# Performance work log

Measured on AMD Instinct MI355X. Metric: run time of the kernel, lower is better.

## Reference

```python
import jax, jax.numpy as jnp
import numpy as np

D = 1024          # d_model / hidden_size
F = 2048          # d_ff / intermediate_size
E = 7             # routed experts = num_experts(8) - num_shared(1)
K = 2             # top_k
AUX_COEF = 0.01


def setup_inputs() -> dict:
    key = jax.random.key(0)
    ks = jax.random.split(key, 6)
    std = 0.02
    x = jax.random.normal(ks[0], (2, 1024, D), dtype=jnp.float32)
    router_w = jax.random.normal(ks[1], (E, D), dtype=jnp.float32) * std      # Linear(D->E), no bias
    cfc_w = jax.random.normal(ks[2], (E, 2 * F, D), dtype=jnp.float32) * std  # fused gate+up per expert
    cproj_w = jax.random.normal(ks[3], (E, D, F), dtype=jnp.float32) * std    # down proj per expert
    shared_fc_w = jax.random.normal(ks[4], (2 * F, D), dtype=jnp.float32) * std
    shared_proj_w = jax.random.normal(ks[5], (D, F), dtype=jnp.float32) * std
    return {"x": x, "router_w": router_w, "cfc_w": cfc_w, "cproj_w": cproj_w,
            "shared_fc_w": shared_fc_w, "shared_proj_w": shared_proj_w}


def reference(x, router_w, cfc_w, cproj_w, shared_fc_w, shared_proj_w):
    b, s, d = x.shape
    T = b * s
    xt = x.reshape(T, d)                                     # [T, D]

    # ---- router: softmax + top-k, renormalized gates ----
    logits = xt @ router_w.T                                 # [T, E]
    probs = jax.nn.softmax(logits, axis=-1)                  # [T, E]
    topv, topi = jax.lax.top_k(probs, K)                     # [T, K]
    gates = topv / jnp.sum(topv, axis=-1, keepdims=True)     # [T, K]
    oh = jax.nn.one_hot(topi, E, dtype=probs.dtype)          # [T, K, E]
    combine = jnp.einsum('tk,tke->te', gates, oh)            # [T, E] sparse combine weights

    # ---- grouped-GEMM SwiGLU experts (dense dispatch over E) ----
    h = jnp.einsum('td,efd->tef', xt, cfc_w)                 # [T, E, 2F]
    g, u = jnp.split(h, 2, axis=-1)                          # [T, E, F] each
    act = jax.nn.silu(g) * u                                 # [T, E, F]
    act = act * combine[..., None]                           # weight before down-proj
    y = jnp.einsum('tef,edf->td', act, cproj_w)              # [T, D]

    # ---- load-balancing aux loss ----
    tokens_per_expert = jnp.mean(jnp.sum(oh, axis=1), axis=0) / K  # [E]
    mean_probs = jnp.mean(probs, axis=0)                            # [E]
    aux = (E * jnp.sum(tokens_per_expert * mean_probs)) * AUX_COEF

    # ---- shared expert (single SwiGLU, num_shared_experts == 1) ----
    hs = xt @ shared_fc_w.T                                  # [T, 2F]
    gs, us = jnp.split(hs, 2, axis=-1)
    shared = (jax.nn.silu(gs) * us) @ shared_proj_w.T        # [T, D]

    y = y + shared
    return y.reshape(b, s, d), aux.astype(x.dtype)
```

## Files before the change

### kernel.cpp

```cpp
#include <hip/hip_runtime.h>

#define TT 2048
#define DM 1024
#define FF 2048
#define NE 7
#define NSLOT 6144
#define H_LD 4096

typedef short bf16x8 __attribute__((ext_vector_type(8)));
typedef float f32x4 __attribute__((ext_vector_type(4)));

__device__ __forceinline__ unsigned short f2bf(float f) {
  union { float f; unsigned int u; } v; v.f = f;
  unsigned int r = v.u + 0x7fffu + ((v.u >> 16) & 1u);
  return (unsigned short)(r >> 16);
}
__device__ __forceinline__ float bf2f(unsigned short s) {
  union { unsigned int u; float f; } v; v.u = ((unsigned int)s) << 16;
  return v.f;
}

__global__ __launch_bounds__(256) void convert_x_kernel(
    const float* __restrict__ x, unsigned short* __restrict__ xb) {
  int i = (blockIdx.x * 256 + threadIdx.x) * 8;
  float4 a = *(const float4*)(x + i);
  float4 b = *(const float4*)(x + i + 4);
  bf16x8 o;
  o[0]=(short)f2bf(a.x); o[1]=(short)f2bf(a.y); o[2]=(short)f2bf(a.z); o[3]=(short)f2bf(a.w);
  o[4]=(short)f2bf(b.x); o[5]=(short)f2bf(b.y); o[6]=(short)f2bf(b.z); o[7]=(short)f2bf(b.w);
  *(bf16x8*)(xb + i) = o;
}

__global__ __launch_bounds__(256) void router_kernel(
    const float* __restrict__ x, const float* __restrict__ rw,
    int* __restrict__ cnt, float* __restrict__ probsum,
    int* __restrict__ idxl, float* __restrict__ gwl) {
  __shared__ float ps[NE];
  int tid = threadIdx.x;
  if (tid < NE) ps[tid] = 0.f;
  __syncthreads();
  int wave = tid >> 6, lane = tid & 63;
  int t = blockIdx.x * 4 + wave;
  float xv[16];
#pragma unroll
  for (int i = 0; i < 16; ++i) xv[i] = x[(size_t)t * DM + lane + i * 64];
  float lg[NE];
#pragma unroll
  for (int e = 0; e < NE; ++e) {
    float s = 0.f;
#pragma unroll
    for (int i = 0; i < 16; ++i) s += xv[i] * rw[e * DM + lane + i * 64];
#pragma unroll
    for (int o = 32; o > 0; o >>= 1) s += __shfl_xor(s, o);
    lg[e] = s;
  }
  float m = lg[0];
#pragma unroll
  for (int e = 1; e < NE; ++e) m = fmaxf(m, lg[e]);
  float p[NE]; float sum = 0.f;
#pragma unroll
  for (int e = 0; e < NE; ++e) { p[e] = expf(lg[e] - m); sum += p[e]; }
  float inv = 1.f / sum;
  int i1 = 0; float v1 = p[0];
#pragma unroll
  for (int e = 1; e < NE; ++e) if (p[e] > v1) { v1 = p[e]; i1 = e; }
  int i2 = -1; float v2 = -1.f;
#pragma unroll
  for (int e = 0; e < NE; ++e) if (e != i1 && p[e] > v2) { v2 = p[e]; i2 = e; }
  float g1 = v1 / (v1 + v2), g2 = v2 / (v1 + v2);
  if (lane == 0) {
#pragma unroll
    for (int e = 0; e < NE; ++e) atomicAdd(&ps[e], p[e] * inv);
    int pos = atomicAdd(&cnt[i1], 1); idxl[i1 * TT + pos] = t; gwl[i1 * TT + pos] = g1;
    pos = atomicAdd(&cnt[i2], 1);     idxl[i2 * TT + pos] = t; gwl[i2 * TT + pos] = g2;
    idxl[NE * TT + t] = t; gwl[NE * TT + t] = 1.0f;
  }
  __syncthreads();
  if (tid < NE) atomicAdd(&probsum[tid], ps[tid]);
}

__global__ void finalize_kernel(int* __restrict__ cnt, int* __restrict__ offs,
                                const float* __restrict__ probsum,
                                float* __restrict__ aux_out) {
  if (threadIdx.x == 0) {
    int o = 0;
    for (int e = 0; e < NE; ++e) { offs[e] = o; o += cnt[e]; }
    offs[NE] = o;
    cnt[NE] = TT;
    double s = 0.0;
    for (int e = 0; e < NE; ++e) s += (double)cnt[e] * (double)probsum[e];
    aux_out[0] = (float)(0.01 * 7.0 * s / (4096.0 * 2048.0));
  }
}

__global__ __launch_bounds__(256) void compact_kernel(
    const int* __restrict__ cnt, const int* __restrict__ offs,
    const int* __restrict__ idxl, const float* __restrict__ gwl,
    int* __restrict__ token_s, float* __restrict__ gate_s) {
  int j = blockIdx.x * 256 + threadIdx.x;
  int e = j >> 11, pos = j & 2047;
  if (pos < cnt[e]) {
    int s = offs[e] + pos;
    token_s[s] = idxl[j];
    gate_s[s] = gwl[j];
  }
}

template <int MODE>
__global__ __launch_bounds__(256) void moe_gemm_kernel(
    const unsigned short* __restrict__ Abase,
    const float* __restrict__ Bw_routed, const float* __restrict__ Bw_shared,
    unsigned short* __restrict__ Hout, float* __restrict__ Yout,
    const int* __restrict__ cnt, const int* __restrict__ offs,
    const int* __restrict__ token_s, int N, int K, int lda) {
  __shared__ unsigned short As[128 * 32];
  __shared__ unsigned short Bs[128 * 32];
  const int e = blockIdx.z;
  const int cnt_e = cnt[e];
  const int m0 = blockIdx.y * 128;
  if (m0 >= cnt_e) return;
  const int off_e = offs[e];
  const int n0 = blockIdx.x * 128;
  const float* Bw = (e == NE) ? Bw_shared : Bw_routed + (size_t)e * N * K;

  const int tid = threadIdx.x;
  const int wave = tid >> 6, lane = tid & 63;

  const int srow = tid >> 1, kh = tid & 1;
  int rr = min(m0 + srow, cnt_e - 1);
  int slot = off_e + rr;
  int arow = (MODE == 0) ? token_s[slot] : slot;
  const unsigned short* ap = Abase + (size_t)arow * lda + kh * 16;
  const float* bp = Bw + (size_t)(n0 + srow) * K + kh * 16;
  unsigned short* adst = &As[srow * 32 + kh * 16];
  unsigned short* bdst = &Bs[srow * 32 + kh * 16];

  f32x4 acc[4][4];
#pragma unroll
  for (int m = 0; m < 4; ++m)
#pragma unroll
    for (int n = 0; n < 4; ++n) acc[m][n] = (f32x4){0.f, 0.f, 0.f, 0.f};

  const int wr = wave >> 1, wc = wave & 1;
  const int lr = lane & 15, lh = lane >> 4;

  for (int k0 = 0; k0 < K; k0 += 32) {
    __syncthreads();
    bf16x8 a0 = *(const bf16x8*)(ap + k0);
    bf16x8 a1 = *(const bf16x8*)(ap + k0 + 8);
    float4 b0 = *(const float4*)(bp + k0);
    float4 b1 = *(const float4*)(bp + k0 + 4);
    float4 b2 = *(const float4*)(bp + k0 + 8);
    float4 b3 = *(const float4*)(bp + k0 + 12);
    *(bf16x8*)adst = a0;
    *(bf16x8*)(adst + 8) = a1;
    bf16x8 w0, w1;
    w0[0]=(short)f2bf(b0.x); w0[1]=(short)f2bf(b0.y); w0[2]=(short)f2bf(b0.z); w0[3]=(short)f2bf(b0.w);
    w0[4]=(short)f2bf(b1.x); w0[5]=(short)f2bf(b1.y); w0[6]=(short)f2bf(b1.z); w0[7]=(short)f2bf(b1.w);
    w1[0]=(short)f2bf(b2.x); w1[1]=(short)f2bf(b2.y); w1[2]=(short)f2bf(b2.z); w1[3]=(short)f2bf(b2.w);
    w1[4]=(short)f2bf(b3.x); w1[5]=(short)f2bf(b3.y); w1[6]=(short)f2bf(b3.z); w1[7]=(short)f2bf(b3.w);
    *(bf16x8*)bdst = w0;
    *(bf16x8*)(bdst + 8) = w1;
    __syncthreads();
    bf16x8 af[4], bfv[4];
#pragma unroll
    for (int m = 0; m < 4; ++m)
      af[m] = *(const bf16x8*)&As[(wr * 64 + m * 16 + lr) * 32 + lh * 8];
#pragma unroll
    for (int n = 0; n < 4; ++n)
      bfv[n] = *(const bf16x8*)&Bs[(wc * 64 + n * 16 + lr) * 32 + lh * 8];
#pragma unroll
    for (int m = 0; m < 4; ++m)
#pragma unroll
      for (int n = 0; n < 4; ++n)
        acc[m][n] = __builtin_amdgcn_mfma_f32_16x16x32_bf16(af[m], bfv[n], acc[m][n], 0, 0, 0);
  }

#pragma unroll
  for (int m = 0; m < 4; ++m) {
#pragma unroll
    for (int j = 0; j < 4; ++j) {
      int r = wr * 64 + m * 16 + lh * 4 + j;
      int gm = m0 + r;
      if (gm < cnt_e) {
        if (MODE == 0) {
          size_t base = (size_t)(off_e + gm) * H_LD + n0;
#pragma unroll
          for (int n = 0; n < 4; ++n)
            Hout[base + wc * 64 + n * 16 + lr] = (unsigned short)(short)f2bf(acc[m][n][j]);
        } else {
          int tok = token_s[off_e + gm];
          size_t base = (size_t)tok * DM + n0;
#pragma unroll
          for (int n = 0; n < 4; ++n)
            atomicAdd(&Yout[base + wc * 64 + n * 16 + lr], acc[m][n][j]);
        }
      }
    }
  }
}

__global__ __launch_bounds__(256) void swiglu_kernel(
    unsigned short* __restrict__ h, const float* __restrict__ gate_s) {
  int slot = blockIdx.x;
  float gate = gate_s[slot];
  unsigned short* row = h + (size_t)slot * H_LD;
  int f0 = threadIdx.x * 8;
  bf16x8 gv = *(const bf16x8*)(row + f0);
  bf16x8 uv = *(const bf16x8*)(row + f0 + FF);
  bf16x8 o;
#pragma unroll
  for (int j = 0; j < 8; ++j) {
    float g = bf2f((unsigned short)gv[j]);
    float u = bf2f((unsigned short)uv[j]);
    float sg = g / (1.f + __expf(-g));
    o[j] = (short)f2bf(sg * u * gate);
  }
  *(bf16x8*)(row + f0) = o;
}

extern "C" void kernel_launch(void* const* d_in, const int* in_sizes, int n_in,
                              void* d_out, int out_size, void* d_ws, size_t ws_size,
                              hipStream_t stream) {
  const float* x     = (const float*)d_in[0];
  const float* rw    = (const float*)d_in[1];
  const float* cfc   = (const float*)d_in[2];
  const float* cproj = (const float*)d_in[3];
  const float* sfc   = (const float*)d_in[4];
  const float* sproj = (const float*)d_in[5];
  float* out = (float*)d_out;

  char* w = (char*)d_ws;
  unsigned short* xb = (unsigned short*)w; w += (size_t)TT * DM * 2;
  unsigned short* h  = (unsigned short*)w; w += (size_t)NSLOT * H_LD * 2;
  int*   idxl    = (int*)w;   w += (size_t)8 * TT * 4;
  float* gwl     = (float*)w; w += (size_t)8 * TT * 4;
  int*   token_s = (int*)w;   w += (size_t)NSLOT * 4;
  float* gate_s  = (float*)w; w += (size_t)NSLOT * 4;
  int*   cnt     = (int*)w;   w += 32;
  float* probsum = (float*)w; w += 32;
  int*   offs    = (int*)w;   w += 32;

  hipMemsetAsync(d_out, 0, (size_t)out_size * sizeof(float), stream);
  hipMemsetAsync(cnt, 0, 64, stream);

  convert_x_kernel<<<1024, 256, 0, stream>>>(x, xb);
  router_kernel<<<512, 256, 0, stream>>>(x, rw, cnt, probsum, idxl, gwl);
  finalize_kernel<<<1, 64, 0, stream>>>(cnt, offs, probsum, out + 2097152);
  compact_kernel<<<64, 256, 0, stream>>>(cnt, offs, idxl, gwl, token_s, gate_s);
  moe_gemm_kernel<0><<<dim3(32, 16, 8), 256, 0, stream>>>(
      xb, cfc, sfc, h, nullptr, cnt, offs, token_s, 4096, 1024, 1024);
  swiglu_kernel<<<NSLOT, 256, 0, stream>>>(h, gate_s);
  moe_gemm_kernel<1><<<dim3(8, 16, 8), 256, 0, stream>>>(
      h, cproj, sproj, nullptr, out, cnt, offs, token_s, 1024, 2048, 4096);
}
```

Baseline: 560.5 us.

## Pre-convert weights to bf16, fuse SwiGLU into up-proj GEMM, use direct-to-LDS loads

Adds a workspace-backed path that converts all expert and shared weights to bf16 up front. The GEMMs then load A and B tiles with global_load_lds instead of converting fp32 weights inside the loop. The up-projection tile now holds matching gate and up rows, so SiLU·up·gate is applied in the epilogue, which removes the separate swiglu pass and halves the intermediate buffer. The cost is an extra full pass over roughly 100MB of fp32 weights on every call, plus narrower per-wave tiles. The old path is kept as a fallback when the workspace is too small.

Result: faster. 466.0 us (-16.9%).

```diff
diff --git a/kernel.cpp b/kernel.cpp
--- a/kernel.cpp
+++ b/kernel.cpp
@@ -20,15 +20,20 @@
   return v.f;
 }
 
-__global__ __launch_bounds__(256) void convert_x_kernel(
-    const float* __restrict__ x, unsigned short* __restrict__ xb) {
-  int i = (blockIdx.x * 256 + threadIdx.x) * 8;
-  float4 a = *(const float4*)(x + i);
-  float4 b = *(const float4*)(x + i + 4);
+#define GLDS16(gp, lp)                                                        \
+  __builtin_amdgcn_global_load_lds(                                           \
+      (const __attribute__((address_space(1))) void*)(gp),                    \
+      (__attribute__((address_space(3))) void*)(lp), 16, 0, 0)
+
+__global__ __launch_bounds__(256) void convert_kernel(
+    const float* __restrict__ src, unsigned short* __restrict__ dst) {
+  size_t i = ((size_t)blockIdx.x * 256 + threadIdx.x) * 8;
+  float4 a = *(const float4*)(src + i);
+  float4 b = *(const float4*)(src + i + 4);
   bf16x8 o;
   o[0]=(short)f2bf(a.x); o[1]=(short)f2bf(a.y); o[2]=(short)f2bf(a.z); o[3]=(short)f2bf(a.w);
   o[4]=(short)f2bf(b.x); o[5]=(short)f2bf(b.y); o[6]=(short)f2bf(b.z); o[7]=(short)f2bf(b.w);
-  *(bf16x8*)(xb + i) = o;
+  *(bf16x8*)(dst + i) = o;
 }
 
 __global__ __launch_bounds__(256) void router_kernel(
@@ -107,7 +112,124 @@
 }
 
 template <int MODE>
-__global__ __launch_bounds__(256) void moe_gemm_kernel(
+__global__ __launch_bounds__(256) void moe_gemm2_kernel(
+    const unsigned short* __restrict__ Abase,
+    const unsigned short* __restrict__ Wb,
+    unsigned short* __restrict__ ActOut, float* __restrict__ Yout,
+    const int* __restrict__ cnt, const int* __restrict__ offs,
+    const int* __restrict__ token_s, const float* __restrict__ gate_s) {
+  constexpr int NB = (MODE == 0) ? 8 : 4;
+  constexpr int BROWS = NB * 16;
+  constexpr int K = (MODE == 0) ? 1024 : 2048;
+  constexpr int LDA = (MODE == 0) ? 1024 : 2048;
+  constexpr int WSTRIDE = (MODE == 0) ? 4096 * 1024 : 1024 * 2048;
+
+  __shared__ unsigned short As[128 * 32];
+  __shared__ unsigned short Bs[BROWS * 32];
+
+  const int e = blockIdx.z;
+  const int cnt_e = cnt[e];
+  const int m0 = blockIdx.y * 128;
+  if (m0 >= cnt_e) return;
+  const int off_e = offs[e];
+  const int nb = blockIdx.x;
+  const unsigned short* Bw = Wb + (size_t)e * WSTRIDE;
+
+  const int tid = threadIdx.x;
+  const int w = tid >> 6, l = tid & 63;
+  const int kq = l & 3;
+  const int lsub = l >> 2;
+
+  const unsigned short* aSrc0;
+  const unsigned short* aSrc1;
+  {
+    int r0 = w * 32 + lsub, r1 = r0 + 16;
+    int rr0 = min(m0 + r0, cnt_e - 1), rr1 = min(m0 + r1, cnt_e - 1);
+    int arow0 = (MODE == 0) ? token_s[off_e + rr0] : (off_e + rr0);
+    int arow1 = (MODE == 0) ? token_s[off_e + rr1] : (off_e + rr1);
+    aSrc0 = Abase + (size_t)arow0 * LDA + kq * 8;
+    aSrc1 = Abase + (size_t)arow1 * LDA + kq * 8;
+  }
+  unsigned short* aDst0 = &As[(w * 32) * 32];
+  unsigned short* aDst1 = &As[(w * 32 + 16) * 32];
+
+  const unsigned short* bSrc0;
+  const unsigned short* bSrc1 = nullptr;
+  unsigned short* bDst0;
+  unsigned short* bDst1 = nullptr;
+  if (MODE == 0) {
+    int r0 = w * 32 + lsub, r1 = r0 + 16;
+    int w0 = (r0 < 64) ? nb * 64 + r0 : 2048 + nb * 64 + (r0 - 64);
+    int w1 = (r1 < 64) ? nb * 64 + r1 : 2048 + nb * 64 + (r1 - 64);
+    bSrc0 = Bw + (size_t)w0 * K + kq * 8;
+    bSrc1 = Bw + (size_t)w1 * K + kq * 8;
+    bDst0 = &Bs[(w * 32) * 32];
+    bDst1 = &Bs[(w * 32 + 16) * 32];
+  } else {
+    int r0 = w * 16 + lsub;
+    bSrc0 = Bw + (size_t)(nb * 64 + r0) * K + kq * 8;
+    bDst0 = &Bs[(w * 16) * 32];
+  }
+
+  f32x4 acc[2][NB];
+#pragma unroll
+  for (int m = 0; m < 2; ++m)
+#pragma unroll
+    for (int n = 0; n < NB; ++n) acc[m][n] = (f32x4){0.f, 0.f, 0.f, 0.f};
+
+  const int lr = l & 15, lh = l >> 4;
+
+  for (int k0 = 0; k0 < K; k0 += 32) {
+    __syncthreads();
+    GLDS16(aSrc0 + k0, aDst0);
+    GLDS16(aSrc1 + k0, aDst1);
+    GLDS16(bSrc0 + k0, bDst0);
+    if (MODE == 0) GLDS16(bSrc1 + k0, bDst1);
+    __syncthreads();
+    bf16x8 af[2], bfv[NB];
+#pragma unroll
+    for (int m = 0; m < 2; ++m)
+      af[m] = *(const bf16x8*)&As[(w * 32 + m * 16 + lr) * 32 + lh * 8];
+#pragma unroll
+    for (int n = 0; n < NB; ++n)
+      bfv[n] = *(const bf16x8*)&Bs[(n * 16 + lr) * 32 + lh * 8];
+#pragma unroll
+    for (int m = 0; m < 2; ++m)
+#pragma unroll
+      for (int n = 0; n < NB; ++n)
+        acc[m][n] = __builtin_amdgcn_mfma_f32_16x16x32_bf16(af[m], bfv[n], acc[m][n], 0, 0, 0);
+  }
+
+#pragma unroll
+  for (int m = 0; m < 2; ++m) {
+#pragma unroll
+    for (int j = 0; j < 4; ++j) {
+      int r = w * 32 + m * 16 + lh * 4 + j;
+      int gm = m0 + r;
+      if (gm < cnt_e) {
+        if (MODE == 0) {
+          float gate = gate_s[off_e + gm];
+          size_t base = (size_t)(off_e + gm) * FF + nb * 64;
+#pragma unroll
+          for (int n = 0; n < 4; ++n) {
+            float g = acc[m][n][j], u = acc[m][n + 4][j];
+            float sg = g / (1.f + __expf(-g));
+            ActOut[base + n * 16 + lr] = f2bf(sg * u * gate);
+          }
+        } else {
+          int tok = token_s[off_e + gm];
+          size_t base = (size_t)tok * DM + nb * 64;
+#pragma unroll
+          for (int n = 0; n < 4; ++n)
+            atomicAdd(&Yout[base + n * 16 + lr], acc[m][n][j]);
+        }
+      }
+    }
+  }
+}
+
+template <int MODE>
+__global__ __launch_bounds__(256) void legacy_gemm_kernel(
     const unsigned short* __restrict__ Abase,
     const float* __restrict__ Bw_routed, const float* __restrict__ Bw_shared,
     unsigned short* __restrict__ Hout, float* __restrict__ Yout,
@@ -122,10 +244,8 @@
   const int off_e = offs[e];
   const int n0 = blockIdx.x * 128;
   const float* Bw = (e == NE) ? Bw_shared : Bw_routed + (size_t)e * N * K;
-
   const int tid = threadIdx.x;
   const int wave = tid >> 6, lane = tid & 63;
-
   const int srow = tid >> 1, kh = tid & 1;
   int rr = min(m0 + srow, cnt_e - 1);
   int slot = off_e + rr;
@@ -134,16 +254,13 @@
   const float* bp = Bw + (size_t)(n0 + srow) * K + kh * 16;
   unsigned short* adst = &As[srow * 32 + kh * 16];
   unsigned short* bdst = &Bs[srow * 32 + kh * 16];
-
   f32x4 acc[4][4];
 #pragma unroll
   for (int m = 0; m < 4; ++m)
 #pragma unroll
     for (int n = 0; n < 4; ++n) acc[m][n] = (f32x4){0.f, 0.f, 0.f, 0.f};
-
   const int wr = wave >> 1, wc = wave & 1;
   const int lr = lane & 15, lh = lane >> 4;
-
   for (int k0 = 0; k0 < K; k0 += 32) {
     __syncthreads();
     bf16x8 a0 = *(const bf16x8*)(ap + k0);
@@ -175,7 +292,6 @@
       for (int n = 0; n < 4; ++n)
         acc[m][n] = __builtin_amdgcn_mfma_f32_16x16x32_bf16(af[m], bfv[n], acc[m][n], 0, 0, 0);
   }
-
 #pragma unroll
   for (int m = 0; m < 4; ++m) {
 #pragma unroll
@@ -200,7 +316,7 @@
   }
 }
 
-__global__ __launch_bounds__(256) void swiglu_kernel(
+__global__ __launch_bounds__(256) void legacy_swiglu_kernel(
     unsigned short* __restrict__ h, const float* __restrict__ gate_s) {
   int slot = blockIdx.x;
   float gate = gate_s[slot];
@@ -230,27 +346,66 @@
   const float* sproj = (const float*)d_in[5];
   float* out = (float*)d_out;
 
-  char* w = (char*)d_ws;
-  unsigned short* xb = (unsigned short*)w; w += (size_t)TT * DM * 2;
-  unsigned short* h  = (unsigned short*)w; w += (size_t)NSLOT * H_LD * 2;
-  int*   idxl    = (int*)w;   w += (size_t)8 * TT * 4;
-  float* gwl     = (float*)w; w += (size_t)8 * TT * 4;
-  int*   token_s = (int*)w;   w += (size_t)NSLOT * 4;
-  float* gate_s  = (float*)w; w += (size_t)NSLOT * 4;
-  int*   cnt     = (int*)w;   w += 32;
-  float* probsum = (float*)w; w += 32;
-  int*   offs    = (int*)w;   w += 32;
+  const size_t SZ_XB  = (size_t)TT * DM * 2;
+  const size_t SZ_WFC = (size_t)8 * 4096 * 1024 * 2;
+  const size_t SZ_WPJ = (size_t)8 * 1024 * 2048 * 2;
+  const size_t SZ_ACT = (size_t)NSLOT * FF * 2;
+  const size_t SZ_LISTS = (size_t)8 * TT * 8 + (size_t)NSLOT * 8 + 384;
+  const size_t need_new = SZ_XB + SZ_WFC + SZ_WPJ + SZ_ACT + SZ_LISTS;
 
   hipMemsetAsync(d_out, 0, (size_t)out_size * sizeof(float), stream);
-  hipMemsetAsync(cnt, 0, 64, stream);
-
-  convert_x_kernel<<<1024, 256, 0, stream>>>(x, xb);
-  router_kernel<<<512, 256, 0, stream>>>(x, rw, cnt, probsum, idxl, gwl);
-  finalize_kernel<<<1, 64, 0, stream>>>(cnt, offs, probsum, out + 2097152);
-  compact_kernel<<<64, 256, 0, stream>>>(cnt, offs, idxl, gwl, token_s, gate_s);
-  moe_gemm_kernel<0><<<dim3(32, 16, 8), 256, 0, stream>>>(
-      xb, cfc, sfc, h, nullptr, cnt, offs, token_s, 4096, 1024, 1024);
-  swiglu_kernel<<<NSLOT, 256, 0, stream>>>(h, gate_s);
-  moe_gemm_kernel<1><<<dim3(8, 16, 8), 256, 0, stream>>>(
-      h, cproj, sproj, nullptr, out, cnt, offs, token_s, 1024, 2048, 4096);
-}
+
+  if (ws_size >= need_new) {
+    char* w = (char*)d_ws;
+    unsigned short* xb    = (unsigned short*)w; w += SZ_XB;
+    unsigned short* wfc_b = (unsigned short*)w; w += SZ_WFC;
+    unsigned short* wpj_b = (unsigned short*)w; w += SZ_WPJ;
+    unsigned short* act   = (unsigned short*)w; w += SZ_ACT;
+    int*   idxl    = (int*)w;   w += (size_t)8 * TT * 4;
+    float* gwl     = (float*)w; w += (size_t)8 * TT * 4;
+    int*   token_s = (int*)w;   w += (size_t)NSLOT * 4;
+    float* gate_s  = (float*)w; w += (size_t)NSLOT * 4;
+    int*   cnt     = (int*)w;   w += 32;
+    float* probsum = (float*)w; w += 32;
+    int*   offs    = (int*)w;   w += 32;
+
+    hipMemsetAsync(cnt, 0, 64, stream);
+
+    convert_kernel<<<1024, 256, 0, stream>>>(x, xb);
+    convert_kernel<<<14336, 256, 0, stream>>>(cfc, wfc_b);
+    convert_kernel<<<2048, 256, 0, stream>>>(sfc, wfc_b + (size_t)7 * 4096 * 1024);
+    convert_kernel<<<7168, 256, 0, stream>>>(cproj, wpj_b);
+    convert_kernel<<<1024, 256, 0, stream>>>(sproj, wpj_b + (size_t)7 * 1024 * 2048);
+
+    router_kernel<<<512, 256, 0, stream>>>(x, rw, cnt, probsum, idxl, gwl);
+    finalize_kernel<<<1, 64, 0, stream>>>(cnt, offs, probsum, out + 2097152);
+    compact_kernel<<<64, 256, 0, stream>>>(cnt, offs, idxl, gwl, token_s, gate_s);
+
+    moe_gemm2_kernel<0><<<dim3(32, 16, 8), 256, 0, stream>>>(
+        xb, wfc_b, act, nullptr, cnt, offs, token_s, gate_s);
+    moe_gemm2_kernel<1><<<dim3(16, 16, 8), 256, 0, stream>>>(
+        act, wpj_b, nullptr, out, cnt, offs, token_s, gate_s);
+  } else {
+    char* w = (char*)d_ws;
+    unsigned short* xb = (unsigned short*)w; w += (size_t)TT * DM * 2;
+    unsigned short* h  = (unsigned short*)w; w += (size_t)NSLOT * H_LD * 2;
+    int*   idxl    = (int*)w;   w += (size_t)8 * TT * 4;
+    float* gwl     = (float*)w; w += (size_t)8 * TT * 4;
+    int*   token_s = (int*)w;   w += (size_t)NSLOT * 4;
+    float* gate_s  = (float*)w; w += (size_t)NSLOT * 4;
+    int*   cnt     = (int*)w;   w += 32;
+    float* probsum = (float*)w; w += 32;
+    int*   offs    = (int*)w;   w += 32;
+
+    hipMemsetAsync(cnt, 0, 64, stream);
+    convert_kernel<<<1024, 256, 0, stream>>>(x, xb);
+    router_kernel<<<512, 256, 0, stream>>>(x, rw, cnt, probsum, idxl, gwl);
+    finalize_kernel<<<1, 64, 0, stream>>>(cnt, offs, probsum, out + 2097152);
+    compact_kernel<<<64, 256, 0, stream>>>(cnt, offs, idxl, gwl, token_s, gate_s);
+    legacy_gemm_kernel<0><<<dim3(32, 16, 8), 256, 0, stream>>>(
+        xb, cfc, sfc, h, nullptr, cnt, offs, token_s, 4096, 1024, 1024);
+    legacy_swiglu_kernel<<<NSLOT, 256, 0, stream>>>(h, gate_s);
+    legacy_gemm_kernel<1><<<dim3(8, 16, 8), 256, 0, stream>>>(
+        h, cproj, sproj, nullptr, out, cnt, offs, token_s, 1024, 2048, 4096);
+  }
+}
```
